# Kernel tuning notes

Hardware: AMD Instinct MI355X
Metric: run time of the kernel (lower is better)

Reference implementation:

```python
import jax, jax.numpy as jnp
import numpy as np

B, N, C = 4, 4096, 1024
H, HC = 16, 64
R = int(HC * np.log(HC))  # 266 random features
EPS = 1e-3


def _orthogonal_projection(num_rows, num_cols, seed=0):
    # Block-orthogonal random matrix: QR of gaussian blocks, rows concatenated.
    rng = np.random.default_rng(seed)
    blocks = []
    n_full = num_rows // num_cols
    for _ in range(n_full):
        q, _ = np.linalg.qr(rng.standard_normal((num_cols, num_cols)))
        blocks.append(q.T)
    remain = num_rows - n_full * num_cols
    if remain > 0:
        q, _ = np.linalg.qr(rng.standard_normal((num_cols, num_cols)))
        blocks.append(q.T[:remain])
    return np.concatenate(blocks, axis=0).astype(np.float32)  # (num_rows, num_cols)


def setup_inputs() -> dict:
    key = jax.random.key(0)
    ks = jax.random.split(key, 6)
    scale = 0.02
    return {
        "x": jax.random.normal(ks[0], (B, N, C), dtype=jnp.float32),
        "Wq": jax.random.normal(ks[1], (C, H * HC), dtype=jnp.float32) * scale,
        "Wk": jax.random.normal(ks[2], (C, H * HC), dtype=jnp.float32) * scale,
        "Wv": jax.random.normal(ks[3], (C, H * HC), dtype=jnp.float32) * scale,
        "Wo": jax.random.normal(ks[4], (H * HC, C), dtype=jnp.float32) * scale,
        "bo": jnp.zeros((C,), dtype=jnp.float32),
        "proj": jnp.asarray(_orthogonal_projection(R, HC, seed=0)),
    }


def reference(x, Wq, Wk, Wv, Wo, bo, proj):
    b, n, _ = x.shape
    # qkv projections, split heads: (B, H, N, HC)
    q = (x @ Wq).reshape(b, n, H, HC).transpose(0, 2, 1, 3)
    k = (x @ Wk).reshape(b, n, H, HC).transpose(0, 2, 1, 3)
    v = (x @ Wv).reshape(b, n, H, HC).transpose(0, 2, 1, 3)
    # FAVOR+ generalized kernel: relu(x @ proj^T) + eps -> (B, H, N, R)
    qp = jax.nn.relu(jnp.einsum('bhnd,rd->bhnr', q, proj)) + EPS
    kp = jax.nn.relu(jnp.einsum('bhnd,rd->bhnr', k, proj)) + EPS
    # linear attention: O(N) in sequence length
    k_sum = kp.sum(axis=-2)                                   # (B, H, R)
    d_inv = 1.0 / jnp.einsum('bhnr,bhr->bhn', qp, k_sum)      # (B, H, N)
    kv = jnp.einsum('bhnr,bhnd->bhrd', kp, v)                 # (B, H, R, HC)
    qkv = jnp.einsum('bhnr,bhrd->bhnd', qp, kv)               # (B, H, N, HC)
    out = qkv * d_inv[..., None]
    # merge heads and output projection
    out = out.transpose(0, 2, 1, 3).reshape(b, n, H * HC)
    return out @ Wo + bo
```

## Files before the change

kernel.cpp:

```cpp
#include <hip/hip_runtime.h>
#include <hip/hip_bf16.h>


typedef __bf16 bf16x8 __attribute__((ext_vector_type(8)));
typedef unsigned short u16x8 __attribute__((ext_vector_type(8)));
typedef float  f32x4  __attribute__((ext_vector_type(4)));

#define EPS_F 1e-3f

__device__ __forceinline__ void gld16(const void* g, void* l) {
  __builtin_amdgcn_global_load_lds(
      (const __attribute__((address_space(1))) void*)g,
      (__attribute__((address_space(3))) void*)l, 16, 0, 0);
}

template <int EPI>
__global__ void __launch_bounds__(512, 2)
gemm256(const __hip_bfloat16* __restrict__ A, long lda,
        const __hip_bfloat16* __restrict__ Bt, long ldb,
        void* __restrict__ Cp, long ldc,
        int Mtiles, int Ntiles, int K, const float* __restrict__ bias) {
  __shared__ __align__(16) char sm[131072];

  const int tid  = threadIdx.x;
  const int lane = tid & 63;
  const int wave = tid >> 6;
  const int wm   = wave >> 2;
  const int wn   = wave & 3;
  const int quad = lane >> 4;
  const int l15  = lane & 15;

  const int nwg = Mtiles * Ntiles;
  const int cpx = nwg >> 3;
  const int bid = blockIdx.x;
  const int wid = (bid & 7) * cpx + (bid >> 3);
  const int nt  = wid / Mtiles;
  const int mt  = wid - nt * Mtiles;
  const long m0 = (long)mt * 256;
  const long n0 = (long)nt * 256;

  const int srow = tid >> 3;
  const int sg   = (tid & 7) ^ (srow & 7);
  const __hip_bfloat16* aS = A  + (m0 + srow) * lda + sg * 8;
  const __hip_bfloat16* bS = Bt + (n0 + srow) * ldb + sg * 8;
  char* smc = (char*)sm;
  const int ldsOff = tid * 16;

  const int aRowB = (wm * 128 + l15) * 128;
  const int bRowB = 32768 + (wn * 64 + l15) * 128;
  const int sw    = (l15 & 7) << 4;
  const int cx0   = (quad * 16) ^ sw;
  const int cx1   = (64 + quad * 16) ^ sw;

  f32x4 acc[8][4] = {};

#define STAGE256(pp, kk)                                                     \
  {                                                                          \
    char* ab = smc + (pp) * 65536;                                           \
    _Pragma("unroll") for (int i = 0; i < 4; ++i) {                          \
      gld16(aS + (long)i * 64 * lda + (kk), ab + i * 8192 + ldsOff);         \
      gld16(bS + (long)i * 64 * ldb + (kk), ab + 32768 + i * 8192 + ldsOff); \
    }                                                                        \
  }

  const int NT = K >> 6;
  STAGE256(0, 0)
  STAGE256(1, 64)
  asm volatile("s_waitcnt vmcnt(8)" ::: "memory");
  __builtin_amdgcn_s_barrier();
  asm volatile("" ::: "memory");

  int p = 0;
  for (int t = 0; t < NT; ++t) {
    const char* base = smc + p * 65536;
    bf16x8 bfr[4][2];
#pragma unroll
    for (int jt = 0; jt < 4; ++jt) {
      bfr[jt][0] = *(const bf16x8*)(base + bRowB + jt * 2048 + cx0);
      bfr[jt][1] = *(const bf16x8*)(base + bRowB + jt * 2048 + cx1);
    }
    __builtin_amdgcn_s_setprio(1);
#pragma unroll
    for (int ih = 0; ih < 2; ++ih) {
      bf16x8 af[4][2];
#pragma unroll
      for (int it = 0; it < 4; ++it) {
        af[it][0] = *(const bf16x8*)(base + aRowB + (ih * 4 + it) * 2048 + cx0);
        af[it][1] = *(const bf16x8*)(base + aRowB + (ih * 4 + it) * 2048 + cx1);
      }
#pragma unroll
      for (int it = 0; it < 4; ++it)
#pragma unroll
        for (int jt = 0; jt < 4; ++jt) {
          acc[ih * 4 + it][jt] = __builtin_amdgcn_mfma_f32_16x16x32_bf16(
              af[it][0], bfr[jt][0], acc[ih * 4 + it][jt], 0, 0, 0);
          acc[ih * 4 + it][jt] = __builtin_amdgcn_mfma_f32_16x16x32_bf16(
              af[it][1], bfr[jt][1], acc[ih * 4 + it][jt], 0, 0, 0);
        }
    }
    __builtin_amdgcn_s_setprio(0);
    __builtin_amdgcn_s_barrier();
    asm volatile("" ::: "memory");
    if (t + 2 < NT) {
      STAGE256(p, (long)(t + 2) * 64)
      asm volatile("s_waitcnt vmcnt(8)" ::: "memory");
    } else {
      asm volatile("s_waitcnt vmcnt(0)" ::: "memory");
    }
    __builtin_amdgcn_s_barrier();
    asm volatile("" ::: "memory");
    p ^= 1;
  }
#undef STAGE256

  if constexpr (EPI == 7) {
    __hip_bfloat16* Cb = (__hip_bfloat16*)Cp;
    const long slab  = (n0 >> 10) * 16777216;
    const long ncol0 = (n0 & 1023) + wn * 64 + l15;
#pragma unroll
    for (int it = 0; it < 8; ++it) {
#pragma unroll
      for (int i = 0; i < 4; ++i) {
        const long gm = m0 + wm * 128 + it * 16 + quad * 4 + i;
        __hip_bfloat16* rowp = Cb + slab + gm * 1024 + ncol0;
#pragma unroll
        for (int jt = 0; jt < 4; ++jt)
          rowp[jt * 16] = (__hip_bfloat16)acc[it][jt][i];
      }
    }
  } else if constexpr (EPI == 5) {
    float* Cf = (float*)Cp;
    float bv[4];
#pragma unroll
    for (int jt = 0; jt < 4; ++jt)
      bv[jt] = bias[n0 + wn * 64 + jt * 16 + l15];
#pragma unroll
    for (int it = 0; it < 8; ++it) {
#pragma unroll
      for (int i = 0; i < 4; ++i) {
        const long gm = m0 + wm * 128 + it * 16 + quad * 4 + i;
        float* rowp = Cf + gm * ldc + n0 + wn * 64 + l15;
#pragma unroll
        for (int jt = 0; jt < 4; ++jt)
          rowp[jt * 16] = acc[it][jt][i] + bv[jt];
      }
    }
  }
}

__global__ void __launch_bounds__(512, 2)
favor_kv(const __hip_bfloat16* __restrict__ Kb,
         const __hip_bfloat16* __restrict__ Vb,
         const __hip_bfloat16* __restrict__ projb_g,
         float* __restrict__ kvp) {
  __shared__ __align__(16) char sm[147456];
  char* Kt = sm;
  char* Pj = sm + 16384;
  char* KP = sm + 53248;
  char* VT = sm + 126976;

  const int tid  = threadIdx.x;
  const int lane = tid & 63;
  const int wave = tid >> 6;
  const int quad = lane >> 4;
  const int l15  = lane & 15;
  const int swL  = (l15 & 7) << 4;

  const int bh   = blockIdx.x & 63;
  const int slab = blockIdx.x >> 6;
  const int b    = bh >> 4, h = bh & 15;
  const long rowbase = (long)b * 4096 + (long)slab * 1024;

  for (int p = 0; p < 5; ++p) {
    const int idx = p * 512 + tid;
    if (idx < 2304) {
      const int r = idx >> 3, g = (idx & 7) ^ (r & 7);
      gld16(projb_g + r * 64 + g * 8, Pj + p * 8192 + tid * 16);
    }
  }
  {
    unsigned short* vth = (unsigned short*)(VT + 64 * 256);
    const unsigned short one_bf = 0x3F80;
    for (int i = tid; i < 2048; i += 512) vth[i] = (i < 128) ? one_bf : 0;
  }

  const int wm1 = wave & 3;
  const int wn1 = wave >> 2;
  const int nJ = (wave < 2) ? 3 : 2;

  f32x4 acc2[3][5] = {};

  for (int t = 0; t < 8; ++t) {
    const long n0 = (long)t * 128;
    __syncthreads();
    {
      const int r = tid >> 3, g = (tid & 7) ^ (r & 7);
      gld16(Kb + (rowbase + n0 + r) * 1024 + h * 64 + g * 8, Kt + tid * 16);
      const int r2 = r + 64, g2 = (tid & 7) ^ (r2 & 7);
      gld16(Kb + (rowbase + n0 + r2) * 1024 + h * 64 + g2 * 8,
            Kt + 8192 + tid * 16);
    }
    u16x8 v0, v1;
    {
      const int nl = tid >> 3, seg = tid & 7;
      v0 = *(const u16x8*)(Vb + (rowbase + n0 + nl) * 1024 + h * 64 + seg * 8);
      v1 = *(const u16x8*)(Vb + (rowbase + n0 + 64 + nl) * 1024 + h * 64 +
                           seg * 8);
    }
    __syncthreads();
    {
      const int nl = tid >> 3, seg = tid & 7;
#pragma unroll
      for (int j = 0; j < 8; ++j) {
        const int d = seg * 8 + j;
        const int s = ((d & 7) ^ ((d >> 3) & 7)) << 4;
        *(unsigned short*)(VT + d * 256 + ((nl * 2) ^ s)) = v0[j];
        *(unsigned short*)(VT + d * 256 + (((nl + 64) * 2) ^ s)) = v1[j];
      }
    }
    f32x4 acc1[2][9] = {};
#pragma unroll
    for (int ks = 0; ks < 2; ++ks) {
      const int cb = ks * 64 + quad * 16;
      bf16x8 af[2];
#pragma unroll
      for (int fm = 0; fm < 2; ++fm)
        af[fm] = *(const bf16x8*)(Kt + (wm1 * 32 + fm * 16 + l15) * 128 +
                                  (cb ^ swL));
      bf16x8 bfr[9];
#pragma unroll
      for (int fn = 0; fn < 9; ++fn)
        bfr[fn] = *(const bf16x8*)(Pj + (wn1 * 144 + fn * 16 + l15) * 128 +
                                   (cb ^ swL));
#pragma unroll
      for (int fm = 0; fm < 2; ++fm)
#pragma unroll
        for (int fn = 0; fn < 9; ++fn)
          acc1[fm][fn] = __builtin_amdgcn_mfma_f32_16x16x32_bf16(
              af[fm], bfr[fn], acc1[fm][fn], 0, 0, 0);
    }
#pragma unroll
    for (int fm = 0; fm < 2; ++fm) {
      const int nb = (wm1 * 32 + fm * 16 + quad * 4) * 2;
#pragma unroll
      for (int fn = 0; fn < 9; ++fn) {
        const int r = wn1 * 144 + fn * 16 + l15;
        const bool ok = (r < 266);
        union { __hip_bfloat16 hh[4]; uint2 u; } pk;
#pragma unroll
        for (int ii = 0; ii < 4; ++ii) {
          float v = acc1[fm][fn][ii];
          v = ok ? (fmaxf(v, 0.f) + EPS_F) : 0.f;
          pk.hh[ii] = (__hip_bfloat16)v;
        }
        *(uint2*)(KP + r * 256 + (nb ^ ((r & 7) << 4))) = pk.u;
      }
    }
    __syncthreads();
#pragma unroll
    for (int ks = 0; ks < 4; ++ks) {
      const int cb = ks * 64 + quad * 16;
      bf16x8 bfr[5];
#pragma unroll
      for (int fd = 0; fd < 5; ++fd) {
        const int d = fd * 16 + l15;
        const int s = ((d & 7) ^ ((d >> 3) & 7)) << 4;
        bfr[fd] = *(const bf16x8*)(VT + d * 256 + (cb ^ s));
      }
#pragma unroll
      for (int j = 0; j < 3; ++j) {
        if (j < nJ) {
          const int r = (wave + 8 * j) * 16 + l15;
          const bf16x8 af =
              *(const bf16x8*)(KP + r * 256 + (cb ^ ((r & 7) << 4)));
#pragma unroll
          for (int fd = 0; fd < 5; ++fd)
            acc2[j][fd] = __builtin_amdgcn_mfma_f32_16x16x32_bf16(
                af, bfr[fd], acc2[j][fd], 0, 0, 0);
        }
      }
    }
  }
  float* dst = kvp + (long)blockIdx.x * 23040;
#pragma unroll
  for (int j = 0; j < 3; ++j) {
    if (j < nJ) {
      const int rb = (wave + 8 * j) * 16 + quad * 4;
#pragma unroll
      for (int fd = 0; fd < 5; ++fd) {
        const int d = fd * 16 + l15;
#pragma unroll
        for (int ii = 0; ii < 4; ++ii)
          dst[(long)(rb + ii) * 80 + d] = acc2[j][fd][ii];
      }
    }
  }
}

__global__ void __launch_bounds__(256)
finalize_kvx2(const float* __restrict__ kvp,
              __hip_bfloat16* __restrict__ kvxb) {
  __shared__ float lds_f[23040];
  const int bh = blockIdx.x, t = threadIdx.x;
  for (int p = 0; p < 90; ++p) {
    const int idx = p * 256 + t;
    float s = 0.f;
#pragma unroll
    for (int sl = 0; sl < 4; ++sl)
      s += kvp[(long)(sl * 64 + bh) * 23040 + idx];
    lds_f[idx] = s;
  }
  __syncthreads();
  for (int p = 0; p < 90; ++p) {
    const int idx = p * 256 + t;
    const int d = idx / 288, r = idx % 288;
    kvxb[(long)bh * 23040 + idx] = (__hip_bfloat16)lds_f[r * 80 + d];
  }
}

__global__ void __launch_bounds__(512, 2)
favor_out(const __hip_bfloat16* __restrict__ Qb,
          const __hip_bfloat16* __restrict__ kvxb_g,
          const __hip_bfloat16* __restrict__ projb_g,
          __hip_bfloat16* __restrict__ outm) {
  __shared__ __align__(16) char sm[160000];
  char* Pj = sm;
  char* KX = sm + 36864;
  char* QP = sm + 84224;

  const int tid  = threadIdx.x;
  const int lane = tid & 63;
  const int wave = tid >> 6;
  const int quad = lane >> 4;
  const int l15  = lane & 15;
  const int swL  = (l15 & 7) << 4;

  const int bh  = blockIdx.x >> 3;
  const int rb8 = blockIdx.x & 7;
  const int b = bh >> 4, h = bh & 15;
  const long rowbase = (long)b * 4096 + (long)rb8 * 512;

  for (int p = 0; p < 5; ++p) {
    const int idx = p * 512 + tid;
    if (idx < 2304) {
      const int r = idx >> 3, g = (idx & 7) ^ (r & 7);
      gld16(projb_g + r * 64 + g * 8, Pj + p * 8192 + tid * 16);
    }
  }
  {
    const __hip_bfloat16* src = kvxb_g + (long)bh * 23040;
#pragma unroll
    for (int p = 0; p < 6; ++p) {
      const int idx = p * 512 + tid;
      if (idx < 2880) {
        const int d = idx / 36, g = idx % 36;
        const bf16x8 v = *(const bf16x8*)(src + d * 288 + g * 8);
        *(bf16x8*)(KX + d * 592 + g * 16) = v;
      }
    }
  }
  __syncthreads();

  const int wm1 = wave >> 2;
  const int wn1 = wave & 3;

  for (int s = 0; s < 4; ++s) {
    const long n0 = (long)s * 128;
    {
      const int r = tid >> 3, g = (tid & 7) ^ (r & 7);
      gld16(Qb + (rowbase + n0 + r) * 1024 + h * 64 + g * 8, QP + tid * 16);
      const int r2 = r + 64, g2 = (tid & 7) ^ (r2 & 7);
      gld16(Qb + (rowbase + n0 + r2) * 1024 + h * 64 + g2 * 8,
            QP + 8192 + tid * 16);
    }
    __syncthreads();
    f32x4 acc1[9][2] = {};
#pragma unroll
    for (int ks = 0; ks < 2; ++ks) {
      const int cb = ks * 64 + quad * 16;
      bf16x8 bfr[2];
#pragma unroll
      for (int fn = 0; fn < 2; ++fn)
        bfr[fn] = *(const bf16x8*)(QP + (wn1 * 32 + fn * 16 + l15) * 128 +
                                   (cb ^ swL));
      bf16x8 af[9];
#pragma unroll
      for (int fm = 0; fm < 9; ++fm)
        af[fm] = *(const bf16x8*)(Pj + (wm1 * 144 + fm * 16 + l15) * 128 +
                                  (cb ^ swL));
#pragma unroll
      for (int fm = 0; fm < 9; ++fm)
#pragma unroll
        for (int fn = 0; fn < 2; ++fn)
          acc1[fm][fn] = __builtin_amdgcn_mfma_f32_16x16x32_bf16(
              af[fm], bfr[fn], acc1[fm][fn], 0, 0, 0);
    }
    __syncthreads();
#pragma unroll
    for (int fm = 0; fm < 9; ++fm) {
      const int r0 = wm1 * 144 + fm * 16 + quad * 4;
#pragma unroll
      for (int fn = 0; fn < 2; ++fn) {
        const int n = wn1 * 32 + fn * 16 + l15;
        union { __hip_bfloat16 hh[4]; uint2 u; } pk;
#pragma unroll
        for (int ii = 0; ii < 4; ++ii) {
          float v = acc1[fm][fn][ii];
          v = (r0 + ii < 266) ? (fmaxf(v, 0.f) + EPS_F) : 0.f;
          pk.hh[ii] = (__hip_bfloat16)v;
        }
        *(uint2*)(QP + n * 592 + r0 * 2) = pk.u;
      }
    }
    __syncthreads();
    f32x4 acc2[5] = {};
#pragma unroll
    for (int ks = 0; ks < 9; ++ks) {
      const int cb = ks * 64 + quad * 16;
      const bf16x8 af = *(const bf16x8*)(QP + (wave * 16 + l15) * 592 + cb);
      bf16x8 bfr[5];
#pragma unroll
      for (int fd = 0; fd < 5; ++fd)
        bfr[fd] = *(const bf16x8*)(KX + (fd * 16 + l15) * 592 + cb);
#pragma unroll
      for (int fd = 0; fd < 5; ++fd)
        acc2[fd] = __builtin_amdgcn_mfma_f32_16x16x32_bf16(af, bfr[fd],
                                                           acc2[fd], 0, 0, 0);
    }
    __syncthreads();
    float* Dsh = (float*)QP;
    if (l15 == 0) {
#pragma unroll
      for (int ii = 0; ii < 4; ++ii)
        Dsh[wave * 16 + quad * 4 + ii] = acc2[4][ii];
    }
    __syncthreads();
#pragma unroll
    for (int ii = 0; ii < 4; ++ii) {
      const int nloc = wave * 16 + quad * 4 + ii;
      const float den = Dsh[nloc];
      const float dinv = (den > 1e-30f) ? (1.f / den) : 0.f;
      __hip_bfloat16* rowp = outm + (rowbase + n0 + nloc) * 1024 + h * 64;
#pragma unroll
      for (int fd = 0; fd < 4; ++fd)
        rowp[fd * 16 + l15] = (__hip_bfloat16)(acc2[fd][ii] * dinv);
    }
    __syncthreads();
  }
}

__global__ void cvt_x(const float* __restrict__ x,
                      __hip_bfloat16* __restrict__ xb) {
  const long i = ((long)blockIdx.x * 256 + threadIdx.x) * 8;
  const float4 f0 = *(const float4*)(x + i);
  const float4 f1 = *(const float4*)(x + i + 4);
  union { __hip_bfloat16 h[8]; uint4 u; } r;
  r.h[0] = (__hip_bfloat16)f0.x; r.h[1] = (__hip_bfloat16)f0.y;
  r.h[2] = (__hip_bfloat16)f0.z; r.h[3] = (__hip_bfloat16)f0.w;
  r.h[4] = (__hip_bfloat16)f1.x; r.h[5] = (__hip_bfloat16)f1.y;
  r.h[6] = (__hip_bfloat16)f1.z; r.h[7] = (__hip_bfloat16)f1.w;
  *(uint4*)(xb + i) = r.u;
}

__global__ void transpose_w4(const float* __restrict__ s0,
                             const float* __restrict__ s1,
                             const float* __restrict__ s2,
                             const float* __restrict__ s3,
                             __hip_bfloat16* __restrict__ dq,
                             __hip_bfloat16* __restrict__ dwo) {
  __shared__ float t[32][33];
  const int z = blockIdx.z;
  const float* src = (z == 0) ? s0 : (z == 1) ? s1 : (z == 2) ? s2 : s3;
  __hip_bfloat16* dst = (z < 3) ? (dq + (long)z * 1048576) : dwo;
  const int k0 = blockIdx.x * 32, n0 = blockIdx.y * 32;
  const int tx = threadIdx.x & 31, ty = threadIdx.x >> 5;
#pragma unroll
  for (int i = 0; i < 4; ++i)
    t[ty + i * 8][tx] = src[(long)(k0 + ty + i * 8) * 1024 + n0 + tx];
  __syncthreads();
#pragma unroll
  for (int i = 0; i < 4; ++i)
    dst[(long)(n0 + ty + i * 8) * 1024 + k0 + tx] =
        (__hip_bfloat16)t[tx][ty + i * 8];
}

__global__ void prep_proj(const float* __restrict__ proj,
                          __hip_bfloat16* __restrict__ projb) {
  const int i = blockIdx.x * 256 + threadIdx.x;
  if (i < 288 * 64) {
    const int r = i >> 6;
    __hip_bfloat16 v = (__hip_bfloat16)0.f;
    if (r < 266) v = (__hip_bfloat16)proj[i];
    projb[i] = v;
  }
}

extern "C" void kernel_launch(void* const* d_in, const int* in_sizes, int n_in,
                              void* d_out, int out_size, void* d_ws,
                              size_t ws_size, hipStream_t stream) {
  const float* x    = (const float*)d_in[0];
  const float* Wq   = (const float*)d_in[1];
  const float* Wk   = (const float*)d_in[2];
  const float* Wv   = (const float*)d_in[3];
  const float* Wo   = (const float*)d_in[4];
  const float* bo   = (const float*)d_in[5];
  const float* proj = (const float*)d_in[6];
  float* out = (float*)d_out;
  char* ws = (char*)d_ws;

  constexpr long o_wqkvt = 0;
  constexpr long o_wot   = 6291456;
  constexpr long o_projb = 8388608;
  constexpr long o_Qb    = 8425472;
  constexpr long o_Kb    = 41979904;
  constexpr long o_Vb    = 75534336;
  constexpr long o_xb    = 109088768;
  constexpr long o_kvp   = 109088768;
  constexpr long o_kvxb  = 132681728;

  __hip_bfloat16* wqkvt = (__hip_bfloat16*)(ws + o_wqkvt);
  __hip_bfloat16* wot   = (__hip_bfloat16*)(ws + o_wot);
  __hip_bfloat16* projb = (__hip_bfloat16*)(ws + o_projb);
  __hip_bfloat16* Qb    = (__hip_bfloat16*)(ws + o_Qb);
  __hip_bfloat16* Kb    = (__hip_bfloat16*)(ws + o_Kb);
  __hip_bfloat16* Vb    = (__hip_bfloat16*)(ws + o_Vb);
  __hip_bfloat16* xb    = (__hip_bfloat16*)(ws + o_xb);
  float*          kvp   = (float*)(ws + o_kvp);
  __hip_bfloat16* kvxb  = (__hip_bfloat16*)(ws + o_kvxb);
  __hip_bfloat16* outm  = Kb;

  cvt_x<<<8192, 256, 0, stream>>>(x, xb);
  transpose_w4<<<dim3(32, 32, 4), 256, 0, stream>>>(Wq, Wk, Wv, Wo, wqkvt,
                                                    wot);
  prep_proj<<<72, 256, 0, stream>>>(proj, projb);

  gemm256<7><<<768, 512, 0, stream>>>(xb, 1024, wqkvt, 1024, Qb, 0, 64, 12,
                                      1024, nullptr);

  favor_kv<<<256, 512, 0, stream>>>(Kb, Vb, projb, kvp);
  finalize_kvx2<<<64, 256, 0, stream>>>(kvp, kvxb);

  favor_out<<<512, 512, 0, stream>>>(Qb, kvxb, projb, outm);

  gemm256<5><<<256, 512, 0, stream>>>(outm, 1024, wot, 1024, out, 1024, 64, 4,
                                      1024, bo);
}
```

Before: 395.3 us.

## Prefetch next K/V and Q tiles into registers and relax barriers

The favor_kv kernel now issues the next tile's K global-to-LDS loads and V register loads right after the mid-loop barrier, so they overlap the KV MFMA accumulation. favor_out preloads the next Q tile into registers during compute and uses raw s_barrier with explicit waitcnt instead of __syncthreads, moving the denominator buffer to its own LDS region to drop two barriers per iteration. The GEMM workgroup-to-tile mapping is also changed to group tiles per XCD for better L2 locality. The cost is more registers held live and hand-managed waitcnt ordering, which raises the risk of races.

```diff
diff --git a/kernel.cpp b/kernel.cpp
--- a/kernel.cpp
+++ b/kernel.cpp
@@ -30,12 +30,15 @@
   const int quad = lane >> 4;
   const int l15  = lane & 15;
 
-  const int nwg = Mtiles * Ntiles;
-  const int cpx = nwg >> 3;
   const int bid = blockIdx.x;
-  const int wid = (bid & 7) * cpx + (bid >> 3);
-  const int nt  = wid / Mtiles;
-  const int mt  = wid - nt * Mtiles;
+  const int Mx  = Mtiles >> 3;
+  const int xcd = bid & 7;
+  const int wl  = bid >> 3;
+  const int gsz = Mx << 2;
+  const int grp = wl / gsz;
+  const int rr  = wl - grp * gsz;
+  const int mt  = xcd * Mx + (rr % Mx);
+  const int nt  = (grp << 2) + (rr / Mx);
   const long m0 = (long)mt * 256;
   const long n0 = (long)nt * 256;
 
@@ -184,6 +187,15 @@
     for (int i = tid; i < 2048; i += 512) vth[i] = (i < 128) ? one_bf : 0;
   }
 
+  const int rS = tid >> 3, gS = (tid & 7) ^ (rS & 7);
+  const int rS2 = rS + 64, gS2 = (tid & 7) ^ (rS2 & 7);
+  const int nl = tid >> 3, seg = tid & 7;
+  gld16(Kb + (rowbase + rS) * 1024 + h * 64 + gS * 8, Kt + tid * 16);
+  gld16(Kb + (rowbase + rS2) * 1024 + h * 64 + gS2 * 8, Kt + 8192 + tid * 16);
+  u16x8 vc0 = *(const u16x8*)(Vb + (rowbase + nl) * 1024 + h * 64 + seg * 8);
+  u16x8 vc1 =
+      *(const u16x8*)(Vb + (rowbase + 64 + nl) * 1024 + h * 64 + seg * 8);
+
   const int wm1 = wave & 3;
   const int wn1 = wave >> 2;
   const int nJ = (wave < 2) ? 3 : 2;
@@ -191,31 +203,16 @@
   f32x4 acc2[3][5] = {};
 
   for (int t = 0; t < 8; ++t) {
-    const long n0 = (long)t * 128;
-    __syncthreads();
+    asm volatile("s_waitcnt vmcnt(0)" ::: "memory");
+    __builtin_amdgcn_s_barrier();
+    asm volatile("" ::: "memory");
     {
-      const int r = tid >> 3, g = (tid & 7) ^ (r & 7);
-      gld16(Kb + (rowbase + n0 + r) * 1024 + h * 64 + g * 8, Kt + tid * 16);
-      const int r2 = r + 64, g2 = (tid & 7) ^ (r2 & 7);
-      gld16(Kb + (rowbase + n0 + r2) * 1024 + h * 64 + g2 * 8,
-            Kt + 8192 + tid * 16);
-    }
-    u16x8 v0, v1;
-    {
-      const int nl = tid >> 3, seg = tid & 7;
-      v0 = *(const u16x8*)(Vb + (rowbase + n0 + nl) * 1024 + h * 64 + seg * 8);
-      v1 = *(const u16x8*)(Vb + (rowbase + n0 + 64 + nl) * 1024 + h * 64 +
-                           seg * 8);
-    }
-    __syncthreads();
-    {
-      const int nl = tid >> 3, seg = tid & 7;
 #pragma unroll
       for (int j = 0; j < 8; ++j) {
         const int d = seg * 8 + j;
         const int s = ((d & 7) ^ ((d >> 3) & 7)) << 4;
-        *(unsigned short*)(VT + d * 256 + ((nl * 2) ^ s)) = v0[j];
-        *(unsigned short*)(VT + d * 256 + (((nl + 64) * 2) ^ s)) = v1[j];
+        *(unsigned short*)(VT + d * 256 + ((nl * 2) ^ s)) = vc0[j];
+        *(unsigned short*)(VT + d * 256 + (((nl + 64) * 2) ^ s)) = vc1[j];
       }
     }
     f32x4 acc1[2][9] = {};
@@ -256,7 +253,19 @@
         *(uint2*)(KP + r * 256 + (nb ^ ((r & 7) << 4))) = pk.u;
       }
     }
-    __syncthreads();
+    asm volatile("s_waitcnt lgkmcnt(0)" ::: "memory");
+    __builtin_amdgcn_s_barrier();
+    asm volatile("" ::: "memory");
+    if (t < 7) {
+      const long n1 = (long)(t + 1) * 128;
+      gld16(Kb + (rowbase + n1 + rS) * 1024 + h * 64 + gS * 8, Kt + tid * 16);
+      gld16(Kb + (rowbase + n1 + rS2) * 1024 + h * 64 + gS2 * 8,
+            Kt + 8192 + tid * 16);
+      vc0 = *(const u16x8*)(Vb + (rowbase + n1 + nl) * 1024 + h * 64 +
+                            seg * 8);
+      vc1 = *(const u16x8*)(Vb + (rowbase + n1 + 64 + nl) * 1024 + h * 64 +
+                            seg * 8);
+    }
 #pragma unroll
     for (int ks = 0; ks < 4; ++ks) {
       const int cb = ks * 64 + quad * 16;
@@ -323,10 +332,11 @@
           const __hip_bfloat16* __restrict__ kvxb_g,
           const __hip_bfloat16* __restrict__ projb_g,
           __hip_bfloat16* __restrict__ outm) {
-  __shared__ __align__(16) char sm[160000];
+  __shared__ __align__(16) char sm[160512];
   char* Pj = sm;
   char* KX = sm + 36864;
   char* QP = sm + 84224;
+  float* Dsh = (float*)(sm + 160000);
 
   const int tid  = threadIdx.x;
   const int lane = tid & 63;
@@ -359,21 +369,21 @@
       }
     }
   }
-  __syncthreads();
+  const int rS = tid >> 3, gS = (tid & 7) ^ (rS & 7);
+  const int rS2 = rS + 64, gS2 = (tid & 7) ^ (rS2 & 7);
+  u16x8 qv0 = *(const u16x8*)(Qb + (rowbase + rS) * 1024 + h * 64 + gS * 8);
+  u16x8 qv1 = *(const u16x8*)(Qb + (rowbase + rS2) * 1024 + h * 64 + gS2 * 8);
 
   const int wm1 = wave >> 2;
   const int wn1 = wave & 3;
 
   for (int s = 0; s < 4; ++s) {
-    const long n0 = (long)s * 128;
-    {
-      const int r = tid >> 3, g = (tid & 7) ^ (r & 7);
-      gld16(Qb + (rowbase + n0 + r) * 1024 + h * 64 + g * 8, QP + tid * 16);
-      const int r2 = r + 64, g2 = (tid & 7) ^ (r2 & 7);
-      gld16(Qb + (rowbase + n0 + r2) * 1024 + h * 64 + g2 * 8,
-            QP + 8192 + tid * 16);
-    }
-    __syncthreads();
+    *(u16x8*)(QP + tid * 16) = qv0;
+    *(u16x8*)(QP + 8192 + tid * 16) = qv1;
+    asm volatile("s_waitcnt lgkmcnt(0)" ::: "memory");
+    if (s == 0) asm volatile("s_waitcnt vmcnt(0)" ::: "memory");
+    __builtin_amdgcn_s_barrier();
+    asm volatile("" ::: "memory");
     f32x4 acc1[9][2] = {};
 #pragma unroll
     for (int ks = 0; ks < 2; ++ks) {
@@ -395,7 +405,14 @@
           acc1[fm][fn] = __builtin_amdgcn_mfma_f32_16x16x32_bf16(
               af[fm], bfr[fn], acc1[fm][fn], 0, 0, 0);
     }
-    __syncthreads();
+    if (s < 3) {
+      const long n1 = (long)(s + 1) * 128;
+      qv0 = *(const u16x8*)(Qb + (rowbase + n1 + rS) * 1024 + h * 64 + gS * 8);
+      qv1 = *(const u16x8*)(Qb + (rowbase + n1 + rS2) * 1024 + h * 64 +
+                            gS2 * 8);
+    }
+    __builtin_amdgcn_s_barrier();
+    asm volatile("" ::: "memory");
 #pragma unroll
     for (int fm = 0; fm < 9; ++fm) {
       const int r0 = wm1 * 144 + fm * 16 + quad * 4;
@@ -412,7 +429,9 @@
         *(uint2*)(QP + n * 592 + r0 * 2) = pk.u;
       }
     }
-    __syncthreads();
+    asm volatile("s_waitcnt lgkmcnt(0)" ::: "memory");
+    __builtin_amdgcn_s_barrier();
+    asm volatile("" ::: "memory");
     f32x4 acc2[5] = {};
 #pragma unroll
     for (int ks = 0; ks < 9; ++ks) {
@@ -427,25 +446,25 @@
         acc2[fd] = __builtin_amdgcn_mfma_f32_16x16x32_bf16(af, bfr[fd],
                                                            acc2[fd], 0, 0, 0);
     }
-    __syncthreads();
-    float* Dsh = (float*)QP;
     if (l15 == 0) {
 #pragma unroll
       for (int ii = 0; ii < 4; ++ii)
         Dsh[wave * 16 + quad * 4 + ii] = acc2[4][ii];
     }
-    __syncthreads();
+    asm volatile("s_waitcnt lgkmcnt(0)" ::: "memory");
+    __builtin_amdgcn_s_barrier();
+    asm volatile("" ::: "memory");
 #pragma unroll
     for (int ii = 0; ii < 4; ++ii) {
       const int nloc = wave * 16 + quad * 4 + ii;
       const float den = Dsh[nloc];
       const float dinv = (den > 1e-30f) ? (1.f / den) : 0.f;
-      __hip_bfloat16* rowp = outm + (rowbase + n0 + nloc) * 1024 + h * 64;
+      __hip_bfloat16* rowp =
+          outm + (rowbase + (long)s * 128 + nloc) * 1024 + h * 64;
 #pragma unroll
       for (int fd = 0; fd < 4; ++fd)
         rowp[fd * 16 + l15] = (__hip_bfloat16)(acc2[fd][ii] * dinv);
     }
-    __syncthreads();
   }
 }
 
```

New measurement: 387.4 us. -2.0%, faster.
